# Kernel optimization log

Measured on AMD Instinct MI355X. Metric: run time of the kernel, lower is better.

The kernel has to match this reference:

```python
import jax, jax.numpy as jnp
import numpy as np

N_EMBD = 1024
HEAD_SIZE = 64
BLOCK = 4096
B = 4

def setup_inputs() -> dict:
    key = jax.random.key(0)
    k1, k2, k3, k4, k5, k6 = jax.random.split(key, 6)
    x = jax.random.normal(k1, (B, BLOCK, N_EMBD), dtype=jnp.float32)
    freqs_cos = jax.random.uniform(k2, (BLOCK, HEAD_SIZE // 2), dtype=jnp.float32)
    freqs_sin = jax.random.uniform(k3, (BLOCK, HEAD_SIZE // 2), dtype=jnp.float32)
    # bias-free Linear weights, stored as [in, out] so y = x @ W
    s = 1.0 / np.sqrt(N_EMBD)
    Wq = jax.random.normal(k4, (N_EMBD, HEAD_SIZE), dtype=jnp.float32) * s
    Wk = jax.random.normal(k5, (N_EMBD, HEAD_SIZE), dtype=jnp.float32) * s
    Wv = jax.random.normal(k6, (N_EMBD, HEAD_SIZE), dtype=jnp.float32) * s
    return {"x": x, "Wq": Wq, "Wk": Wk, "Wv": Wv,
            "freqs_cos": freqs_cos, "freqs_sin": freqs_sin}

def _rope(t, cos, sin):
    # t: [B,T,hs]; cos/sin: [T, hs//2]. Rotate consecutive (even,odd) pairs.
    tr = t[..., 0::2]
    ti = t[..., 1::2]
    cos = cos[None, :, :]
    sin = sin[None, :, :]
    out_r = tr * cos - ti * sin
    out_i = tr * sin + ti * cos
    return jnp.stack([out_r, out_i], axis=-1).reshape(t.shape)

def reference(x, Wq, Wk, Wv, freqs_cos, freqs_sin):
    B_, T, C = x.shape
    q = x @ Wq  # [B,T,hs]
    k = x @ Wk
    v = x @ Wv
    q = _rope(q, freqs_cos[:T], freqs_sin[:T])
    k = _rope(k, freqs_cos[:T], freqs_sin[:T])
    scale = k.shape[-1] ** -0.5
    wei = jnp.einsum('bqd,bkd->bqk', q, k) * scale  # [B,T,T]
    mask = jnp.tril(jnp.ones((T, T), dtype=bool))
    wei = jnp.where(mask[None], wei, -jnp.inf)
    wei = jax.nn.softmax(wei, axis=-1)
    return jnp.einsum('bqk,bkd->bqd', wei, v)
```

## Files before the change

kernel.cpp:

```cpp
#include <hip/hip_runtime.h>
#include <hip/hip_bf16.h>
#include <stdint.h>

#define TSEQ 4096
#define CEMB 1024
#define DH   64
#define NB   4
#define NCHUNK 4

typedef __attribute__((ext_vector_type(8))) short bf16x8;
typedef __attribute__((ext_vector_type(4))) float f32x4;
typedef __attribute__((ext_vector_type(4))) float f4;
typedef unsigned short u16;

__device__ __forceinline__ u16 f2bf(float f) {
  __hip_bfloat16 h = __float2bfloat16(f);
  return *(u16*)&h;
}

__device__ __forceinline__ int swz(int row, int colbyte) {
  return row * 128 + (colbyte ^ ((row & 7) << 4));
}

__global__ void prep_w(const float* __restrict__ Wq, const float* __restrict__ Wk,
                       const float* __restrict__ Wv, u16* __restrict__ wt) {
  int idx = blockIdx.x * 256 + threadIdx.x;
  if (idx >= 3 * DH * CEMB) return;
  int m = idx >> 16;
  int r = idx & 65535;
  int k = r >> 6, n = r & 63;
  const float* W = (m == 0) ? Wq : (m == 1) ? Wk : Wv;
  wt[(size_t)m * 65536 + n * 1024 + k] = f2bf(W[r]);
}

#define QKV_LOADX(K0) { \
    const float* s_ = x + (size_t)(m0 + xrow) * CEMB + (K0) + xc * 8; \
    xa = *(const f4*)s_; xb = *(const f4*)(s_ + 4); }
#define QKV_LOADW(K0) \
    _Pragma("unroll") for (int it = 0; it < 6; ++it) { \
      int gg = it * 256 + tid; \
      wv[it] = *(const bf16x8*)(wt + (size_t)(gg >> 3) * CEMB + (K0) + (gg & 7) * 8); }
#define QKV_STORE(BUF) { \
    bf16x8 xv_; \
    xv_[0] = (short)f2bf(xa[0]); xv_[1] = (short)f2bf(xa[1]); \
    xv_[2] = (short)f2bf(xa[2]); xv_[3] = (short)f2bf(xa[3]); \
    xv_[4] = (short)f2bf(xb[0]); xv_[5] = (short)f2bf(xb[1]); \
    xv_[6] = (short)f2bf(xb[2]); xv_[7] = (short)f2bf(xb[3]); \
    *(bf16x8*)((char*)xs[BUF] + swz(xrow, xc << 4)) = xv_; \
    _Pragma("unroll") for (int it = 0; it < 6; ++it) { \
      int gg = it * 256 + tid; \
      *(bf16x8*)((char*)wsh[BUF] + swz(gg >> 3, (gg & 7) << 4)) = wv[it]; } }

__launch_bounds__(256)
__global__ void qkv_gemm(const float* __restrict__ x, const u16* __restrict__ wt,
                         const float* __restrict__ fc, const float* __restrict__ fs,
                         u16* __restrict__ q_ws, u16* __restrict__ k_ws,
                         u16* __restrict__ vt_ws) {
  __shared__ __align__(16) u16 xs[2][32 * 64];
  __shared__ __align__(16) u16 wsh[2][192 * 64];

  const int tid  = threadIdx.x;
  const int lane = tid & 63;
  const int w    = tid >> 6;
  const int l15  = lane & 15;
  const int lhi  = lane >> 4;
  const int rg   = w & 1;
  const int cg   = w >> 1;
  const int m0   = blockIdx.x * 32;
  const int xrow = tid >> 3, xc = tid & 7;

  const f32x4 z4 = {0.f, 0.f, 0.f, 0.f};
  f32x4 acc[6];
#pragma unroll
  for (int j = 0; j < 6; ++j) acc[j] = z4;

  f4 xa, xb;
  bf16x8 wv[6];

  QKV_LOADX(0)
  QKV_LOADW(0)
  QKV_STORE(0)
  __syncthreads();

  for (int ks = 0; ks < CEMB / 64; ++ks) {
    const int cur  = ks & 1;
    const bool more = (ks + 1 < CEMB / 64);
    if (more) {
      QKV_LOADX((ks + 1) * 64)
      QKV_LOADW((ks + 1) * 64)
    }
#pragma unroll
    for (int kk = 0; kk < 2; ++kk) {
      bf16x8 af = *(const bf16x8*)((char*)xs[cur] + swz(rg * 16 + l15, (kk * 32 + lhi * 8) * 2));
#pragma unroll
      for (int nc = 0; nc < 6; ++nc) {
        bf16x8 bfr = *(const bf16x8*)((char*)wsh[cur] + swz(cg * 96 + nc * 16 + l15, (kk * 32 + lhi * 8) * 2));
        acc[nc] = __builtin_amdgcn_mfma_f32_16x16x32_bf16(af, bfr, acc[nc], 0, 0, 0);
      }
    }
    if (more) QKV_STORE(cur ^ 1)
    __syncthreads();
  }

#pragma unroll
  for (int nc = 0; nc < 6; ++nc) {
    int gcol = cg * 96 + nc * 16 + l15;
    int mat  = gcol >> 6;
    int col  = gcol & 63;
#pragma unroll
    for (int r = 0; r < 4; ++r) {
      float v = acc[nc][r];
      float o = __shfl_xor(v, 1);
      int row = m0 + rg * 16 + lhi * 4 + r;
      int b = row >> 12, t = row & 4095;
      if (mat == 2) {
        vt_ws[((size_t)(b * DH + col)) * TSEQ + t] = f2bf(v);
      } else {
        int p = col >> 1;
        float cv = fc[t * 32 + p], sv = fs[t * 32 + p];
        float outv = ((col & 1) == 0) ? (v * cv - o * sv)
                                      : (o * sv + v * cv);
        if (mat == 0) outv *= 0.125f;
        u16* dst = (mat == 0) ? q_ws : k_ws;
        dst[(size_t)row * DH + col] = f2bf(outv);
      }
    }
  }
}

#define ATT_LOADKV(KV0) \
    _Pragma("unroll") for (int it = 0; it < 2; ++it) { \
      int gg = it * 256 + tid, row_ = gg >> 3, cc_ = gg & 7; \
      kreg[it] = *(const bf16x8*)(kb + (size_t)((KV0) + row_) * DH + cc_ * 8); \
      vreg[it] = *(const bf16x8*)(vb + (size_t)row_ * TSEQ + (KV0) + cc_ * 8); }
#define ATT_WRITEKV \
    _Pragma("unroll") for (int it = 0; it < 2; ++it) { \
      int gg = it * 256 + tid, row_ = gg >> 3, cc_ = gg & 7; \
      *(bf16x8*)((char*)kt + swz(row_, cc_ << 4)) = kreg[it]; \
      *(bf16x8*)((char*)vts + swz(row_, cc_ << 4)) = vreg[it]; }

__launch_bounds__(256)
__global__ void attn_partial(const u16* __restrict__ q_ws, const u16* __restrict__ k_ws,
                             const u16* __restrict__ vt_ws, float* __restrict__ po,
                             float* __restrict__ pml) {
  const int qt = blockIdx.x;
  const int b  = blockIdx.y;
  const int c  = blockIdx.z;

  const int ntiles = qt + 1;
  const int cnt    = (ntiles + NCHUNK - 1) / NCHUNK;
  const int t0     = c * cnt;
  if (t0 >= ntiles) return;
  const int t1     = min(t0 + cnt, ntiles);

  __shared__ __align__(16) u16 kt[64 * 64];
  __shared__ __align__(16) u16 vts[64 * 64];
  __shared__ __align__(16) u16 pt2[4 * 16 * 64];

  const int tid  = threadIdx.x;
  const int lane = tid & 63;
  const int w    = tid >> 6;
  const int l15  = lane & 15;
  const int lhi  = lane >> 4;
  const int q0   = qt * 64;

  const u16* qb = q_ws + (size_t)b * TSEQ * DH;
  const u16* kb = k_ws + (size_t)b * TSEQ * DH;
  const u16* vb = vt_ws + (size_t)b * DH * TSEQ;
  char* ptw = (char*)pt2 + w * 2048;

  bf16x8 aq[2];
  {
    int qrow = q0 + w * 16 + l15;
#pragma unroll
    for (int kk = 0; kk < 2; ++kk)
      aq[kk] = *(const bf16x8*)(qb + (size_t)qrow * DH + kk * 32 + lhi * 8);
  }

  const f32x4 z4 = {0.f, 0.f, 0.f, 0.f};
  f32x4 oacc[4] = {z4, z4, z4, z4};
  float m_r[4], l_p[4];
#pragma unroll
  for (int r = 0; r < 4; ++r) { m_r[r] = -1e30f; l_p[r] = 0.f; }

  const int myqbase = q0 + w * 16 + lhi * 4;

  bf16x8 kreg[2], vreg[2];

  for (int kv = t0; kv < t1; ++kv) {
    const int kv0 = kv * 64;
    ATT_LOADKV(kv0)
    __syncthreads();
    ATT_WRITEKV
    __syncthreads();

    f32x4 sacc[4] = {z4, z4, z4, z4};
    __builtin_amdgcn_s_setprio(1);
#pragma unroll
    for (int kk = 0; kk < 2; ++kk) {
#pragma unroll
      for (int cb = 0; cb < 4; ++cb) {
        bf16x8 bk = *(const bf16x8*)((char*)kt + swz(cb * 16 + l15, (kk * 32 + lhi * 8) * 2));
        sacc[cb] = __builtin_amdgcn_mfma_f32_16x16x32_bf16(aq[kk], bk, sacc[cb], 0, 0, 0);
      }
    }
    __builtin_amdgcn_s_setprio(0);

    if (kv0 == q0) {
#pragma unroll
      for (int cb = 0; cb < 4; ++cb)
#pragma unroll
        for (int r = 0; r < 4; ++r) {
          int ki = kv0 + cb * 16 + l15;
          int qi = myqbase + r;
          if (ki > qi) sacc[cb][r] = -1e30f;
        }
    }
    float mx[4];
#pragma unroll
    for (int r = 0; r < 4; ++r)
      mx[r] = fmaxf(fmaxf(sacc[0][r], sacc[1][r]), fmaxf(sacc[2][r], sacc[3][r]));
#pragma unroll
    for (int s = 1; s <= 8; s <<= 1)
#pragma unroll
      for (int r = 0; r < 4; ++r) mx[r] = fmaxf(mx[r], __shfl_xor(mx[r], s));
    bool skip = true;
#pragma unroll
    for (int r = 0; r < 4; ++r) skip = skip && (mx[r] <= m_r[r] + 8.f);
    if (!__all(skip)) {
#pragma unroll
      for (int r = 0; r < 4; ++r) {
        float mn = fmaxf(m_r[r], mx[r]);
        float fac = __expf(m_r[r] - mn);
        m_r[r] = mn;
        l_p[r] *= fac;
#pragma unroll
        for (int nc = 0; nc < 4; ++nc) oacc[nc][r] *= fac;
      }
    }
#pragma unroll
    for (int cb = 0; cb < 4; ++cb)
#pragma unroll
      for (int r = 0; r < 4; ++r) {
        float p = __expf(sacc[cb][r] - m_r[r]);
        l_p[r] += p;
        *(u16*)(ptw + swz(lhi * 4 + r, (cb * 16 + l15) * 2)) = f2bf(p);
      }
    bf16x8 ap[2];
#pragma unroll
    for (int kk = 0; kk < 2; ++kk)
      ap[kk] = *(const bf16x8*)(ptw + swz(l15, (kk * 32 + lhi * 8) * 2));
    __builtin_amdgcn_s_setprio(1);
#pragma unroll
    for (int kk = 0; kk < 2; ++kk)
#pragma unroll
      for (int nc = 0; nc < 4; ++nc) {
        bf16x8 bv = *(const bf16x8*)((char*)vts + swz(nc * 16 + l15, (kk * 32 + lhi * 8) * 2));
        oacc[nc] = __builtin_amdgcn_mfma_f32_16x16x32_bf16(ap[kk], bv, oacc[nc], 0, 0, 0);
      }
    __builtin_amdgcn_s_setprio(0);
  }

#pragma unroll
  for (int s = 1; s <= 8; s <<= 1)
#pragma unroll
    for (int r = 0; r < 4; ++r) l_p[r] += __shfl_xor(l_p[r], s);

  const int slot = ((b * 64 + qt) * NCHUNK + c);
  float* o_out = po + (size_t)slot * (64 * 64);
#pragma unroll
  for (int nc = 0; nc < 4; ++nc)
#pragma unroll
    for (int r = 0; r < 4; ++r) {
      int rloc = w * 16 + lhi * 4 + r;
      o_out[rloc * 64 + nc * 16 + l15] = oacc[nc][r];
    }
#pragma unroll
  for (int r = 0; r < 4; ++r) {
    if (l15 == 0) {
      int rloc = w * 16 + lhi * 4 + r;
      pml[(size_t)slot * 128 + rloc]      = m_r[r];
      pml[(size_t)slot * 128 + 64 + rloc] = l_p[r];
    }
  }
}

__launch_bounds__(256)
__global__ void attn_combine(const float* __restrict__ po, const float* __restrict__ pml,
                             float* __restrict__ out) {
  int idx = blockIdx.x * 256 + threadIdx.x;
  int d   = idx & 63;
  int t   = (idx >> 6) & 4095;
  int b   = idx >> 18;
  int qt  = t >> 6;
  int rloc = t & 63;
  int ntiles = qt + 1;
  int cnt = (ntiles + NCHUNK - 1) / NCHUNK;

  float m_c[NCHUNK], l_c[NCHUNK], o_c[NCHUNK];
  float M = -1e30f;
#pragma unroll
  for (int c = 0; c < NCHUNK; ++c) {
    bool valid = (c * cnt < ntiles);
    int slot = ((b * 64 + qt) * NCHUNK + c);
    m_c[c] = valid ? pml[(size_t)slot * 128 + rloc]      : -1e30f;
    l_c[c] = valid ? pml[(size_t)slot * 128 + 64 + rloc] : 0.f;
    o_c[c] = valid ? po[(size_t)slot * (64 * 64) + rloc * 64 + d] : 0.f;
    M = fmaxf(M, m_c[c]);
  }
  float den = 0.f, num = 0.f;
#pragma unroll
  for (int c = 0; c < NCHUNK; ++c) {
    float e = __expf(m_c[c] - M);
    den += e * l_c[c];
    num += e * o_c[c];
  }
  out[idx] = num / den;
}

extern "C" void kernel_launch(void* const* d_in, const int* in_sizes, int n_in,
                              void* d_out, int out_size, void* d_ws, size_t ws_size,
                              hipStream_t stream) {
  const float* x  = (const float*)d_in[0];
  const float* Wq = (const float*)d_in[1];
  const float* Wk = (const float*)d_in[2];
  const float* Wv = (const float*)d_in[3];
  const float* fc = (const float*)d_in[4];
  const float* fs = (const float*)d_in[5];
  float* out = (float*)d_out;

  char* ws = (char*)d_ws;
  u16*   wt    = (u16*)(ws);
  u16*   q_ws  = (u16*)(ws + (1u << 19));
  u16*   k_ws  = (u16*)(ws + (1u << 19) + (1u << 21));
  u16*   vt_ws = (u16*)(ws + (1u << 19) + (2u << 21));
  float* po    = (float*)(ws + (1u << 19) + (3u << 21));
  float* pml   = (float*)(ws + (1u << 19) + (3u << 21) + (1u << 24));

  prep_w<<<(3 * DH * CEMB + 255) / 256, 256, 0, stream>>>(Wq, Wk, Wv, wt);
  qkv_gemm<<<dim3(512), 256, 0, stream>>>(x, wt, fc, fs, q_ws, k_ws, vt_ws);
  attn_partial<<<dim3(64, NB, NCHUNK), 256, 0, stream>>>(q_ws, k_ws, vt_ws, po, pml);
  attn_combine<<<dim3((NB * TSEQ * DH) / 256), 256, 0, stream>>>(po, pml, out);
}
```

Baseline: 170.1 us.

## Load QKV GEMM operands directly from global and reorder attention block scheduling

The QKV projection no longer stages x and the bf16 weights through double-buffered shared memory. Each lane now loads its MFMA fragments straight from global memory, which removes the shared-memory writes and the per-step barriers but gives up coalesced tile loads and relies on the caches for weight reuse. Separately, attention blocks are relaid onto a 2D grid, and odd chunk indices walk the query tiles in reverse. The goal is to interleave long causal rows with short ones so work is spread more evenly across CUs.

```diff
diff --git a/kernel.cpp b/kernel.cpp
--- a/kernel.cpp
+++ b/kernel.cpp
@@ -33,32 +33,11 @@
   wt[(size_t)m * 65536 + n * 1024 + k] = f2bf(W[r]);
 }
 
-#define QKV_LOADX(K0) { \
-    const float* s_ = x + (size_t)(m0 + xrow) * CEMB + (K0) + xc * 8; \
-    xa = *(const f4*)s_; xb = *(const f4*)(s_ + 4); }
-#define QKV_LOADW(K0) \
-    _Pragma("unroll") for (int it = 0; it < 6; ++it) { \
-      int gg = it * 256 + tid; \
-      wv[it] = *(const bf16x8*)(wt + (size_t)(gg >> 3) * CEMB + (K0) + (gg & 7) * 8); }
-#define QKV_STORE(BUF) { \
-    bf16x8 xv_; \
-    xv_[0] = (short)f2bf(xa[0]); xv_[1] = (short)f2bf(xa[1]); \
-    xv_[2] = (short)f2bf(xa[2]); xv_[3] = (short)f2bf(xa[3]); \
-    xv_[4] = (short)f2bf(xb[0]); xv_[5] = (short)f2bf(xb[1]); \
-    xv_[6] = (short)f2bf(xb[2]); xv_[7] = (short)f2bf(xb[3]); \
-    *(bf16x8*)((char*)xs[BUF] + swz(xrow, xc << 4)) = xv_; \
-    _Pragma("unroll") for (int it = 0; it < 6; ++it) { \
-      int gg = it * 256 + tid; \
-      *(bf16x8*)((char*)wsh[BUF] + swz(gg >> 3, (gg & 7) << 4)) = wv[it]; } }
-
 __launch_bounds__(256)
 __global__ void qkv_gemm(const float* __restrict__ x, const u16* __restrict__ wt,
                          const float* __restrict__ fc, const float* __restrict__ fs,
                          u16* __restrict__ q_ws, u16* __restrict__ k_ws,
                          u16* __restrict__ vt_ws) {
-  __shared__ __align__(16) u16 xs[2][32 * 64];
-  __shared__ __align__(16) u16 wsh[2][192 * 64];
-
   const int tid  = threadIdx.x;
   const int lane = tid & 63;
   const int w    = tid >> 6;
@@ -67,39 +46,35 @@
   const int rg   = w & 1;
   const int cg   = w >> 1;
   const int m0   = blockIdx.x * 32;
-  const int xrow = tid >> 3, xc = tid & 7;
+
+  const float* xr = x + (size_t)(m0 + rg * 16 + l15) * CEMB;
+  const u16*   wb = wt + (size_t)(cg * 96 + l15) * CEMB;
 
   const f32x4 z4 = {0.f, 0.f, 0.f, 0.f};
   f32x4 acc[6];
 #pragma unroll
   for (int j = 0; j < 6; ++j) acc[j] = z4;
 
-  f4 xa, xb;
-  bf16x8 wv[6];
-
-  QKV_LOADX(0)
-  QKV_LOADW(0)
-  QKV_STORE(0)
-  __syncthreads();
-
-  for (int ks = 0; ks < CEMB / 64; ++ks) {
-    const int cur  = ks & 1;
-    const bool more = (ks + 1 < CEMB / 64);
-    if (more) {
-      QKV_LOADX((ks + 1) * 64)
-      QKV_LOADW((ks + 1) * 64)
-    }
+#pragma unroll 2
+  for (int k0 = 0; k0 < CEMB; k0 += 64) {
+    bf16x8 af[2];
 #pragma unroll
     for (int kk = 0; kk < 2; ++kk) {
-      bf16x8 af = *(const bf16x8*)((char*)xs[cur] + swz(rg * 16 + l15, (kk * 32 + lhi * 8) * 2));
+      const float* s = xr + k0 + kk * 32 + lhi * 8;
+      f4 a = *(const f4*)s;
+      f4 b = *(const f4*)(s + 4);
+      af[kk][0] = (short)f2bf(a[0]); af[kk][1] = (short)f2bf(a[1]);
+      af[kk][2] = (short)f2bf(a[2]); af[kk][3] = (short)f2bf(a[3]);
+      af[kk][4] = (short)f2bf(b[0]); af[kk][5] = (short)f2bf(b[1]);
+      af[kk][6] = (short)f2bf(b[2]); af[kk][7] = (short)f2bf(b[3]);
+    }
+#pragma unroll
+    for (int kk = 0; kk < 2; ++kk)
 #pragma unroll
       for (int nc = 0; nc < 6; ++nc) {
-        bf16x8 bfr = *(const bf16x8*)((char*)wsh[cur] + swz(cg * 96 + nc * 16 + l15, (kk * 32 + lhi * 8) * 2));
-        acc[nc] = __builtin_amdgcn_mfma_f32_16x16x32_bf16(af, bfr, acc[nc], 0, 0, 0);
-      }
-    }
-    if (more) QKV_STORE(cur ^ 1)
-    __syncthreads();
+        bf16x8 bfr = *(const bf16x8*)(wb + (size_t)nc * 16 * CEMB + k0 + kk * 32 + lhi * 8);
+        acc[nc] = __builtin_amdgcn_mfma_f32_16x16x32_bf16(af[kk], bfr, acc[nc], 0, 0, 0);
+      }
   }
 
 #pragma unroll
@@ -143,9 +118,12 @@
 __global__ void attn_partial(const u16* __restrict__ q_ws, const u16* __restrict__ k_ws,
                              const u16* __restrict__ vt_ws, float* __restrict__ po,
                              float* __restrict__ pml) {
-  const int qt = blockIdx.x;
-  const int b  = blockIdx.y;
-  const int c  = blockIdx.z;
+  const int g  = blockIdx.x;
+  const int j  = blockIdx.y;
+  const int b  = g >> 6;
+  const int r0 = g & 63;
+  const int qt = (j & 1) ? (63 - r0) : r0;
+  const int c  = j;
 
   const int ntiles = qt + 1;
   const int cnt    = (ntiles + NCHUNK - 1) / NCHUNK;
@@ -339,6 +317,6 @@
 
   prep_w<<<(3 * DH * CEMB + 255) / 256, 256, 0, stream>>>(Wq, Wk, Wv, wt);
   qkv_gemm<<<dim3(512), 256, 0, stream>>>(x, wt, fc, fs, q_ws, k_ws, vt_ws);
-  attn_partial<<<dim3(64, NB, NCHUNK), 256, 0, stream>>>(q_ws, k_ws, vt_ws, po, pml);
+  attn_partial<<<dim3(256, NCHUNK), 256, 0, stream>>>(q_ws, k_ws, vt_ws, po, pml);
   attn_combine<<<dim3((NB * TSEQ * DH) / 256), 256, 0, stream>>>(po, pml, out);
 }
```

Result: slower. 192.7 us (+13.3%).
